# Performance work log

Measured on AMD Instinct MI355X. Metric: run time of the kernel, lower is better.

## Reference

```python
import jax, jax.numpy as jnp
import numpy as np

B, CIN, COUT, H, W = 4, 256, 256, 64, 64


def setup_inputs() -> dict:
    key = jax.random.key(0)
    ks = jax.random.split(key, 7)
    x = jax.random.normal(ks[0], (B, CIN, H, W), dtype=jnp.float32)
    s = 1.0 / np.sqrt(CIN)
    Wq = jax.random.uniform(ks[1], (COUT, CIN), jnp.float32, -s, s)
    Wk = jax.random.uniform(ks[2], (COUT, CIN), jnp.float32, -s, s)
    Wv = jax.random.uniform(ks[3], (COUT, CIN), jnp.float32, -s, s)
    bq = jax.random.uniform(ks[4], (COUT,), jnp.float32, -s, s)
    bk = jax.random.uniform(ks[5], (COUT,), jnp.float32, -s, s)
    bv = jax.random.uniform(ks[6], (COUT,), jnp.float32, -s, s)
    return {"x": x, "Wq": Wq, "Wk": Wk, "Wv": Wv, "bq": bq, "bk": bk, "bv": bv}


def reference(x, Wq, Wk, Wv, bq, bk, bv):
    b, cin, h, w = x.shape
    xf = x.reshape(b, cin, h * w)  # [B, Cin, N]
    # 1x1 conv == channel matmul
    q = jnp.einsum('oc,bcn->bon', Wq, xf) + bq[None, :, None]  # [B, C, N]
    k = jnp.einsum('oc,bcn->bon', Wk, xf) + bk[None, :, None]
    v = jnp.einsum('oc,bcn->bon', Wv, xf) + bv[None, :, None]
    # attention over flattened spatial positions (no 1/sqrt(d) scaling, as in source)
    scores = jnp.einsum('bcn,bcm->bnm', q, k)          # [B, N, N]
    attn = jax.nn.softmax(scores, axis=-1)
    out = jnp.einsum('bnm,bcm->bcn', attn, v)          # [B, C, N]
    return out.reshape(b, q.shape[1], h, w)
```

## Files before the change

### kernel.cpp

```cpp
#include <hip/hip_runtime.h>


typedef _Float16 f16;
typedef f16 f16x4 __attribute__((ext_vector_type(4)));
typedef f16 f16x8 __attribute__((ext_vector_type(8)));
typedef float f32x16 __attribute__((ext_vector_type(16)));

#define NB 4
#define NC 256
#define NN 4096
#define KVSPLIT 4
#define KRANGE (NN / KVSPLIT)
#define NCHUNK (KRANGE / 32)

typedef const __attribute__((address_space(1))) void* gas_t;
typedef __attribute__((address_space(3))) void* las_t;

__device__ __forceinline__ void load_lds16(const void* g, void* l) {
    __builtin_amdgcn_global_load_lds((gas_t)g, (las_t)l, 16, 0, 0);
}

__global__ __launch_bounds__(256) void wcvt_kernel(
    const float* __restrict__ Wq, const float* __restrict__ Wk,
    const float* __restrict__ Wv, f16* __restrict__ Wh)
{
    const int idx = blockIdx.x * 256 + threadIdx.x;
    const float* s = (idx < 65536) ? Wq : (idx < 131072 ? Wk : Wv);
    Wh[idx] = (f16)s[idx & 65535];
}

__global__ __launch_bounds__(256) void qkv_mfma_kernel(
    const float* __restrict__ x, const f16* __restrict__ Wh,
    const float* __restrict__ bq, const float* __restrict__ bk, const float* __restrict__ bv,
    f16* __restrict__ Qh, f16* __restrict__ Kh, f16* __restrict__ Vt)
{
    const int b  = blockIdx.y;
    const int n0 = blockIdx.x * 64;
    const int t  = threadIdx.x;
    const int wv = t >> 6, l = t & 63, ln = l & 31, g = l >> 5;

    __shared__ char xs[64 * 512];
    __shared__ char st[32768];

    {
        const int ci0 = t >> 4;
        const int nq  = (t & 15) * 4;
        for (int it = 0; it < 16; ++it) {
            const int ci = it * 16 + ci0;
            float v4[4];
            *(float4*)v4 = *(const float4*)(x + ((size_t)b * NC + ci) * NN + n0 + nq);
            const int gr = ci >> 3, lo = (ci & 7) * 2;
            #pragma unroll
            for (int j = 0; j < 4; ++j) {
                const int n = nq + j;
                *(f16*)(xs + n * 512 + ((gr ^ (n & 7)) * 16 + lo)) = (f16)v4[j];
            }
        }
    }
    __syncthreads();

    const int c0 = wv * 64;
    for (int m = 0; m < 3; ++m) {
        const f16*  W    = Wh + m * (NC * NC);
        const float* bias = (m == 0) ? bq : (m == 1 ? bk : bv);

        f32x16 acc[2][2];
        #pragma unroll
        for (int i = 0; i < 2; ++i)
            #pragma unroll
            for (int j = 0; j < 2; ++j)
                #pragma unroll
                for (int r = 0; r < 16; ++r) acc[i][j][r] = 0.0f;

        #pragma unroll
        for (int cs = 0; cs < 16; ++cs) {
            f16x8 a0 = *(const f16x8*)(W + (size_t)(c0 + ln) * NC + cs * 16 + 8 * g);
            f16x8 a1 = *(const f16x8*)(W + (size_t)(c0 + 32 + ln) * NC + cs * 16 + 8 * g);
            const int xb = (cs * 32 + g * 16) ^ ((ln & 7) << 4);
            f16x8 b0 = *(const f16x8*)(xs + ln * 512 + xb);
            f16x8 b1 = *(const f16x8*)(xs + (32 + ln) * 512 + xb);
            acc[0][0] = __builtin_amdgcn_mfma_f32_32x32x16_f16(a0, b0, acc[0][0], 0, 0, 0);
            acc[0][1] = __builtin_amdgcn_mfma_f32_32x32x16_f16(a0, b1, acc[0][1], 0, 0, 0);
            acc[1][0] = __builtin_amdgcn_mfma_f32_32x32x16_f16(a1, b0, acc[1][0], 0, 0, 0);
            acc[1][1] = __builtin_amdgcn_mfma_f32_32x32x16_f16(a1, b1, acc[1][1], 0, 0, 0);
        }

        __syncthreads();
        if (m < 2) {
            #pragma unroll
            for (int ct = 0; ct < 2; ++ct)
                #pragma unroll
                for (int nt = 0; nt < 2; ++nt)
                    #pragma unroll
                    for (int q = 0; q < 4; ++q) {
                        const int cb = c0 + ct * 32 + 8 * q + 4 * g;
                        f16x4 pk;
                        #pragma unroll
                        for (int j = 0; j < 4; ++j)
                            pk[j] = (f16)(acc[ct][nt][q * 4 + j] + bias[cb + j]);
                        const int n  = nt * 32 + ln;
                        const int g8 = cb >> 3;
                        *(f16x4*)(st + n * 512 + ((g8 ^ (n & 7)) * 16 + (cb & 7) * 2)) = pk;
                    }
            __syncthreads();
            f16* dst = (m == 0) ? Qh : Kh;
            const int gi  = t & 31;
            const int nb8 = (t >> 5) * 8;
            #pragma unroll
            for (int k = 0; k < 8; ++k) {
                const int n = nb8 + k;
                const uint4 d = *(const uint4*)(st + n * 512 + ((gi ^ (n & 7)) << 4));
                *(uint4*)(dst + ((size_t)b * NN + n0 + n) * NC + gi * 8) = d;
            }
        } else {
            #pragma unroll
            for (int ct = 0; ct < 2; ++ct)
                #pragma unroll
                for (int nt = 0; nt < 2; ++nt) {
                    const int n  = nt * 32 + ln;
                    const int pn = (n & ~15) | (n & 3) | ((n & 8) >> 1) | ((n & 4) << 1);
                    #pragma unroll
                    for (int r = 0; r < 16; ++r) {
                        const int c = c0 + ct * 32 + (r & 3) + 8 * (r >> 2) + 4 * g;
                        *(f16*)(st + c * 128 + ((pn * 2) ^ ((c & 7) << 4))) =
                            (f16)(acc[ct][nt][r] + bias[c]);
                    }
                }
            __syncthreads();
            #pragma unroll
            for (int ci = 0; ci < 8; ++ci) {
                const int c = ci * 32 + (t >> 3);
                const int s = t & 7;
                const uint4 d = *(const uint4*)(st + c * 128 + ((s ^ (c & 7)) << 4));
                *(uint4*)(Vt + ((size_t)b * NC + c) * NN + n0 + s * 8) = d;
            }
        }
    }
}

__global__ __launch_bounds__(256, 2) void flash_mfma_kernel(
    const f16* __restrict__ Qh, const f16* __restrict__ Kh, const f16* __restrict__ Vt,
    f16* __restrict__ Op, float* __restrict__ Mst, float* __restrict__ Lst)
{
    const int t  = threadIdx.x;
    const int wv = t >> 6;
    const int l  = t & 63;
    const int ln = l & 31;
    const int g  = l >> 5;

    const int flat  = blockIdx.x;
    const int xcd   = flat & 7;
    const int idx   = flat >> 3;
    const int bs    = xcd * 2 + (idx & 1);
    const int qt    = idx >> 1;
    const int b     = bs >> 2;
    const int split = bs & 3;
    const int qrow  = qt * 128 + wv * 32 + ln;

    __shared__ char ldsK[2 * 16384];
    __shared__ char ldsV[2 * 16384];

    f16x8 qf[16];
    {
        const f16* Qb = Qh + ((size_t)b * NN + qrow) * NC;
        #pragma unroll
        for (int cs = 0; cs < 16; ++cs)
            qf[cs] = *(const f16x8*)(Qb + cs * 16 + 8 * g);
    }

    f32x16 o[8];
    #pragma unroll
    for (int ct = 0; ct < 8; ++ct)
        #pragma unroll
        for (int r = 0; r < 16; ++r) o[ct][r] = 0.0f;

    float mrun = -1e30f, lrun = 0.0f;
    const int key_base = split * KRANGE;
    const f16* KhB = Kh + (size_t)b * NN * NC;
    const f16* VtB = Vt + (size_t)b * NC * NN;

#define DMA(CH, BUF) do {                                                            \
        const int key0_ = key_base + (CH) * 32;                                      \
        _Pragma("unroll")                                                            \
        for (int j = 0; j < 4; ++j) {                                                \
            const int r2  = wv * 4 + j;                                              \
            const int row = r2 * 2 + (l >> 5);                                       \
            const int u   = (l & 31) ^ (row & 15);                                   \
            load_lds16(KhB + (size_t)(key0_ + row) * NC + u * 8,                     \
                       ldsK + (BUF) * 16384 + r2 * 1024);                            \
        }                                                                            \
        _Pragma("unroll")                                                            \
        for (int j = 0; j < 4; ++j) {                                                \
            const int i  = wv * 4 + j;                                               \
            const int R  = i * 4 + (l >> 4);                                         \
            const int c  = R * 4 + ((l & 15) >> 2);                                  \
            const int kg = (l & 3) ^ (R & 3);                                        \
            load_lds16(VtB + (size_t)c * NN + key0_ + kg * 8,                        \
                       ldsV + (BUF) * 16384 + i * 1024);                             \
        }                                                                            \
    } while (0)

    DMA(0, 0);

    for (int ch = 0; ch < NCHUNK; ++ch) {
        const int cb = ch & 1;
        if (ch + 1 < NCHUNK) {
            DMA(ch + 1, cb ^ 1);
            asm volatile("s_waitcnt vmcnt(8)" ::: "memory");
        } else {
            asm volatile("s_waitcnt vmcnt(0)" ::: "memory");
        }
        __builtin_amdgcn_s_barrier();

        const char* K0 = ldsK + cb * 16384;
        const char* V0 = ldsV + cb * 16384;

        f32x16 s0;
        #pragma unroll
        for (int r = 0; r < 16; ++r) s0[r] = 0.0f;
        __builtin_amdgcn_s_setprio(1);
        #pragma unroll
        for (int cs = 0; cs < 16; ++cs) {
            const int col = ((cs * 2 + g) ^ (ln & 15)) * 16;
            f16x8 a0 = *(const f16x8*)(K0 + ln * 512 + col);
            s0 = __builtin_amdgcn_mfma_f32_32x32x16_f16(a0, qf[cs], s0, 0, 0, 0);
        }
        __builtin_amdgcn_s_setprio(0);

        float mt = s0[0];
        #pragma unroll
        for (int r = 1; r < 16; ++r) mt = fmaxf(mt, s0[r]);
        mt = fmaxf(mt, __shfl_xor(mt, 32));
        if (!__all(mt <= mrun + 8.0f)) {
            const float mnew  = fmaxf(mrun, mt);
            const float alpha = __expf(mrun - mnew);
            #pragma unroll
            for (int ct = 0; ct < 8; ++ct)
                #pragma unroll
                for (int r = 0; r < 16; ++r) o[ct][r] *= alpha;
            lrun *= alpha;
            mrun  = mnew;
        }

        float ps = 0.0f;
        f16x8 pf[2];
        #pragma unroll
        for (int r = 0; r < 16; ++r) {
            const float e0 = __expf(s0[r] - mrun);
            ps += e0;
            pf[r >> 3][r & 7] = (f16)e0;
        }
        ps += __shfl_xor(ps, 32);
        lrun += ps;

        __builtin_amdgcn_s_setprio(1);
        #pragma unroll
        for (int ct = 0; ct < 8; ++ct) {
            const int c    = ct * 32 + ln;
            const int base = (c >> 2) * 256 + (c & 3) * 64;
            const int rsw  = (c >> 2) & 3;
            #pragma unroll
            for (int s = 0; s < 2; ++s) {
                f16x8 va = *(const f16x8*)(V0 + base + (((s * 2 + g) ^ rsw) * 16));
                o[ct] = __builtin_amdgcn_mfma_f32_32x32x16_f16(va, pf[s], o[ct], 0, 0, 0);
            }
        }
        __builtin_amdgcn_s_setprio(0);

        __builtin_amdgcn_s_barrier();
    }
#undef DMA

    const float invl = 1.0f / lrun;
    #pragma unroll
    for (int ct = 0; ct < 8; ++ct)
        #pragma unroll
        for (int r = 0; r < 16; ++r) {
            const int c = ct * 32 + (r & 3) + 8 * (r >> 2) + 4 * g;
            Op[((size_t)(split * NB + b) * NC + c) * NN + qrow] = (f16)(o[ct][r] * invl);
        }
    if (g == 0) {
        Mst[(split * NB + b) * NN + qrow] = mrun;
        Lst[(split * NB + b) * NN + qrow] = lrun;
    }
}

__global__ __launch_bounds__(256) void combine_kernel(
    const f16* __restrict__ Op, const float* __restrict__ Mst, const float* __restrict__ Lst,
    float* __restrict__ out)
{
    const int t = threadIdx.x;
    const int b = blockIdx.y;
    const int n = blockIdx.x * 64 + (t & 63);

    float w[KVSPLIT];
    float mm = -1e30f;
    #pragma unroll
    for (int s = 0; s < KVSPLIT; ++s) {
        w[s] = Mst[(s * NB + b) * NN + n];
        mm = fmaxf(mm, w[s]);
    }
    float tot = 0.0f;
    #pragma unroll
    for (int s = 0; s < KVSPLIT; ++s) {
        w[s] = __expf(w[s] - mm) * Lst[(s * NB + b) * NN + n];
        tot += w[s];
    }
    const float inv = 1.0f / tot;
    #pragma unroll
    for (int s = 0; s < KVSPLIT; ++s) w[s] *= inv;

    for (int c = (t >> 6); c < NC; c += 4) {
        float acc = 0.0f;
        #pragma unroll
        for (int s = 0; s < KVSPLIT; ++s)
            acc += w[s] * (float)Op[((size_t)(s * NB + b) * NC + c) * NN + n];
        out[((size_t)b * NC + c) * NN + n] = acc;
    }
}

extern "C" void kernel_launch(void* const* d_in, const int* in_sizes, int n_in,
                              void* d_out, int out_size, void* d_ws, size_t ws_size,
                              hipStream_t stream)
{
    const float* x  = (const float*)d_in[0];
    const float* Wq = (const float*)d_in[1];
    const float* Wk = (const float*)d_in[2];
    const float* Wv = (const float*)d_in[3];
    const float* bq = (const float*)d_in[4];
    const float* bk = (const float*)d_in[5];
    const float* bv = (const float*)d_in[6];
    float* out = (float*)d_out;

    f16* Qh = (f16*)d_ws;
    f16* Kh = Qh + (size_t)NB * NN * NC;
    f16* Vt = Kh + (size_t)NB * NN * NC;
    f16* Op = Vt + (size_t)NB * NN * NC;
    float* Mst = (float*)(Op + (size_t)KVSPLIT * NB * NC * NN);
    float* Lst = Mst + (size_t)KVSPLIT * NB * NN;
    f16*  Wh  = (f16*)(Lst + (size_t)KVSPLIT * NB * NN);

    wcvt_kernel<<<768, 256, 0, stream>>>(Wq, Wk, Wv, Wh);
    qkv_mfma_kernel<<<dim3(NN / 64, NB), 256, 0, stream>>>(
        x, Wh, bq, bk, bv, Qh, Kh, Vt);
    flash_mfma_kernel<<<512, 256, 0, stream>>>(Qh, Kh, Vt, Op, Mst, Lst);
    combine_kernel<<<dim3(NN / 64, NB), 256, 0, stream>>>(Op, Mst, Lst, out);
}
```

Measured before the change: 136.0 us.

## Software-pipeline QK^T one chunk ahead of softmax/PV and use exp2 with prescaled Q

Restructures the attention main loop so the QK^T MFMAs for the next chunk are issued alongside the softmax and PV of the current chunk, using two score accumulators and split K/V DMA issue points. Separately folds log2(e) into Q during projection so the softmax uses exp2f instead of __expf, with the lazy-rescale threshold widened to 12 in the log2 domain. The combine kernel also switches to exp2f to match. The cost is higher register pressure from the extra score accumulator, and fp16 Q values are now scaled by 1.44, which slightly changes rounding.

```diff
diff --git a/kernel.cpp b/kernel.cpp
--- a/kernel.cpp
+++ b/kernel.cpp
@@ -63,6 +63,7 @@
     for (int m = 0; m < 3; ++m) {
         const f16*  W    = Wh + m * (NC * NC);
         const float* bias = (m == 0) ? bq : (m == 1 ? bk : bv);
+        const float qs   = (m == 0) ? 1.44269504f : 1.0f;
 
         f32x16 acc[2][2];
         #pragma unroll
@@ -97,7 +98,7 @@
                         f16x4 pk;
                         #pragma unroll
                         for (int j = 0; j < 4; ++j)
-                            pk[j] = (f16)(acc[ct][nt][q * 4 + j] + bias[cb + j]);
+                            pk[j] = (f16)((acc[ct][nt][q * 4 + j] + bias[cb + j]) * qs);
                         const int n  = nt * 32 + ln;
                         const int g8 = cb >> 3;
                         *(f16x4*)(st + n * 512 + ((g8 ^ (n & 7)) * 16 + (cb & 7) * 2)) = pk;
@@ -175,11 +176,12 @@
         for (int r = 0; r < 16; ++r) o[ct][r] = 0.0f;
 
     float mrun = -1e30f, lrun = 0.0f;
+    f16x8 pf[2];
     const int key_base = split * KRANGE;
     const f16* KhB = Kh + (size_t)b * NN * NC;
     const f16* VtB = Vt + (size_t)b * NC * NN;
 
-#define DMA(CH, BUF) do {                                                            \
+#define KDMA(CH, BUF) do {                                                           \
         const int key0_ = key_base + (CH) * 32;                                      \
         _Pragma("unroll")                                                            \
         for (int j = 0; j < 4; ++j) {                                                \
@@ -189,6 +191,10 @@
             load_lds16(KhB + (size_t)(key0_ + row) * NC + u * 8,                     \
                        ldsK + (BUF) * 16384 + r2 * 1024);                            \
         }                                                                            \
+    } while (0)
+
+#define VDMA(CH, BUF) do {                                                           \
+        const int key0_ = key_base + (CH) * 32;                                      \
         _Pragma("unroll")                                                            \
         for (int j = 0; j < 4; ++j) {                                                \
             const int i  = wv * 4 + j;                                               \
@@ -200,76 +206,96 @@
         }                                                                            \
     } while (0)
 
-    DMA(0, 0);
-
-    for (int ch = 0; ch < NCHUNK; ++ch) {
-        const int cb = ch & 1;
-        if (ch + 1 < NCHUNK) {
-            DMA(ch + 1, cb ^ 1);
-            asm volatile("s_waitcnt vmcnt(8)" ::: "memory");
-        } else {
-            asm volatile("s_waitcnt vmcnt(0)" ::: "memory");
-        }
-        __builtin_amdgcn_s_barrier();
-
-        const char* K0 = ldsK + cb * 16384;
-        const char* V0 = ldsV + cb * 16384;
-
-        f32x16 s0;
-        #pragma unroll
-        for (int r = 0; r < 16; ++r) s0[r] = 0.0f;
-        __builtin_amdgcn_s_setprio(1);
-        #pragma unroll
-        for (int cs = 0; cs < 16; ++cs) {
-            const int col = ((cs * 2 + g) ^ (ln & 15)) * 16;
-            f16x8 a0 = *(const f16x8*)(K0 + ln * 512 + col);
-            s0 = __builtin_amdgcn_mfma_f32_32x32x16_f16(a0, qf[cs], s0, 0, 0, 0);
-        }
-        __builtin_amdgcn_s_setprio(0);
-
-        float mt = s0[0];
-        #pragma unroll
-        for (int r = 1; r < 16; ++r) mt = fmaxf(mt, s0[r]);
-        mt = fmaxf(mt, __shfl_xor(mt, 32));
-        if (!__all(mt <= mrun + 8.0f)) {
-            const float mnew  = fmaxf(mrun, mt);
-            const float alpha = __expf(mrun - mnew);
-            #pragma unroll
-            for (int ct = 0; ct < 8; ++ct)
-                #pragma unroll
-                for (int r = 0; r < 16; ++r) o[ct][r] *= alpha;
-            lrun *= alpha;
-            mrun  = mnew;
-        }
-
-        float ps = 0.0f;
-        f16x8 pf[2];
-        #pragma unroll
-        for (int r = 0; r < 16; ++r) {
-            const float e0 = __expf(s0[r] - mrun);
-            ps += e0;
-            pf[r >> 3][r & 7] = (f16)e0;
-        }
-        ps += __shfl_xor(ps, 32);
-        lrun += ps;
-
-        __builtin_amdgcn_s_setprio(1);
-        #pragma unroll
-        for (int ct = 0; ct < 8; ++ct) {
-            const int c    = ct * 32 + ln;
-            const int base = (c >> 2) * 256 + (c & 3) * 64;
-            const int rsw  = (c >> 2) & 3;
-            #pragma unroll
-            for (int s = 0; s < 2; ++s) {
-                f16x8 va = *(const f16x8*)(V0 + base + (((s * 2 + g) ^ rsw) * 16));
-                o[ct] = __builtin_amdgcn_mfma_f32_32x32x16_f16(va, pf[s], o[ct], 0, 0, 0);
-            }
-        }
-        __builtin_amdgcn_s_setprio(0);
-
-        __builtin_amdgcn_s_barrier();
-    }
-#undef DMA
+#define QKC(BUF, SACC) do {                                                          \
+        _Pragma("unroll")                                                            \
+        for (int r = 0; r < 16; ++r) SACC[r] = 0.0f;                                 \
+        const char* K0_ = ldsK + (BUF) * 16384;                                      \
+        _Pragma("unroll")                                                            \
+        for (int cs = 0; cs < 16; ++cs) {                                            \
+            const int col = ((cs * 2 + g) ^ (ln & 15)) * 16;                         \
+            f16x8 a0 = *(const f16x8*)(K0_ + ln * 512 + col);                        \
+            SACC = __builtin_amdgcn_mfma_f32_32x32x16_f16(a0, qf[cs], SACC, 0, 0, 0);\
+        }                                                                            \
+    } while (0)
+
+#define SM(SP) do {                                                                  \
+        float mt = SP[0];                                                            \
+        _Pragma("unroll")                                                            \
+        for (int r = 1; r < 16; ++r) mt = fmaxf(mt, SP[r]);                          \
+        mt = fmaxf(mt, __shfl_xor(mt, 32));                                          \
+        if (!__all(mt <= mrun + 12.0f)) {                                            \
+            const float mnew  = fmaxf(mrun, mt);                                     \
+            const float alpha = exp2f(mrun - mnew);                                  \
+            _Pragma("unroll")                                                        \
+            for (int ct = 0; ct < 8; ++ct)                                           \
+                _Pragma("unroll")                                                    \
+                for (int r = 0; r < 16; ++r) o[ct][r] *= alpha;                      \
+            lrun *= alpha;                                                           \
+            mrun  = mnew;                                                            \
+        }                                                                            \
+        float ps = 0.0f;                                                             \
+        _Pragma("unroll")                                                            \
+        for (int r = 0; r < 16; ++r) {                                               \
+            const float e0 = exp2f(SP[r] - mrun);                                    \
+            ps += e0;                                                                \
+            pf[r >> 3][r & 7] = (f16)e0;                                             \
+        }                                                                            \
+        ps += __shfl_xor(ps, 32);                                                    \
+        lrun += ps;                                                                  \
+    } while (0)
+
+#define PVC(BUF) do {                                                                \
+        const char* V0_ = ldsV + (BUF) * 16384;                                      \
+        __builtin_amdgcn_s_setprio(1);                                               \
+        _Pragma("unroll")                                                            \
+        for (int ct = 0; ct < 8; ++ct) {                                             \
+            const int c    = ct * 32 + ln;                                           \
+            const int base = (c >> 2) * 256 + (c & 3) * 64;                          \
+            const int rsw  = (c >> 2) & 3;                                           \
+            _Pragma("unroll")                                                        \
+            for (int s = 0; s < 2; ++s) {                                            \
+                f16x8 va = *(const f16x8*)(V0_ + base + (((s * 2 + g) ^ rsw) * 16)); \
+                o[ct] = __builtin_amdgcn_mfma_f32_32x32x16_f16(va, pf[s], o[ct], 0, 0, 0); \
+            }                                                                        \
+        }                                                                            \
+        __builtin_amdgcn_s_setprio(0);                                               \
+    } while (0)
+
+#define STEP(SP, SC, BI, CH, PREF, DOQK, VM4) do {                                   \
+        if (VM4) asm volatile("s_waitcnt vmcnt(4)" ::: "memory");                    \
+        else     asm volatile("s_waitcnt vmcnt(0)" ::: "memory");                    \
+        __builtin_amdgcn_s_barrier();                                                \
+        if (PREF) KDMA((CH) + 2, BI);                                                \
+        if (DOQK) QKC((BI) ^ 1, SC);                                                 \
+        SM(SP);                                                                      \
+        PVC(BI);                                                                     \
+        __builtin_amdgcn_s_barrier();                                                \
+        if (PREF) VDMA((CH) + 2, BI);                                                \
+    } while (0)
+
+    f32x16 sA, sB;
+
+    KDMA(0, 0);
+    VDMA(0, 0);
+    KDMA(1, 1);
+    asm volatile("s_waitcnt vmcnt(8)" ::: "memory");
+    __builtin_amdgcn_s_barrier();
+    QKC(0, sA);
+    VDMA(1, 1);
+
+    for (int it = 0; it < NCHUNK - 2; it += 2) {
+        STEP(sA, sB, 0, it,     1, 1, 1);
+        STEP(sB, sA, 1, it + 1, 1, 1, 1);
+    }
+    STEP(sA, sB, 0, NCHUNK - 2, 0, 1, 1);
+    STEP(sB, sA, 1, NCHUNK - 1, 0, 0, 0);
+
+#undef STEP
+#undef PVC
+#undef SM
+#undef QKC
+#undef VDMA
+#undef KDMA
 
     const float invl = 1.0f / lrun;
     #pragma unroll
@@ -303,7 +329,7 @@
     float tot = 0.0f;
     #pragma unroll
     for (int s = 0; s < KVSPLIT; ++s) {
-        w[s] = __expf(w[s] - mm) * Lst[(s * NB + b) * NN + n];
+        w[s] = exp2f(w[s] - mm) * Lst[(s * NB + b) * NN + n];
         tot += w[s];
     }
     const float inv = 1.0f / tot;
```

New measurement: 248.4 us. +82.6%, slower.

## Fold log2e into Q, use exp2 softmax, split score accumulators, defer row-sum shuffle

Applied to the files above, without the earlier changes.

Scales Q by log2(e) in the projection epilogue so the attention softmax and the split combine can use exp2 directly instead of __expf. The QK^T MFMA chain is split into two independent accumulators to break the serial dependency, and the row max uses a tree reduction. The per-chunk cross-lane shuffle for the row sum is moved to a single shuffle after the loop, and the rescale threshold is widened from 8 to 12 in log2 units. The wider threshold lets unrescaled exponents grow larger before renormalisation, which raises fp16 overflow risk in P.

```diff
diff --git a/kernel.cpp b/kernel.cpp
--- a/kernel.cpp
+++ b/kernel.cpp
@@ -63,6 +63,7 @@
     for (int m = 0; m < 3; ++m) {
         const f16*  W    = Wh + m * (NC * NC);
         const float* bias = (m == 0) ? bq : (m == 1 ? bk : bv);
+        const float qs   = (m == 0) ? 1.44269504f : 1.0f;
 
         f32x16 acc[2][2];
         #pragma unroll
@@ -97,7 +98,7 @@
                         f16x4 pk;
                         #pragma unroll
                         for (int j = 0; j < 4; ++j)
-                            pk[j] = (f16)(acc[ct][nt][q * 4 + j] + bias[cb + j]);
+                            pk[j] = (f16)((acc[ct][nt][q * 4 + j] + bias[cb + j]) * qs);
                         const int n  = nt * 32 + ln;
                         const int g8 = cb >> 3;
                         *(f16x4*)(st + n * 512 + ((g8 ^ (n & 7)) * 16 + (cb & 7) * 2)) = pk;
@@ -215,25 +216,37 @@
         const char* K0 = ldsK + cb * 16384;
         const char* V0 = ldsV + cb * 16384;
 
-        f32x16 s0;
-        #pragma unroll
-        for (int r = 0; r < 16; ++r) s0[r] = 0.0f;
+        f32x16 sa, sb;
+        #pragma unroll
+        for (int r = 0; r < 16; ++r) { sa[r] = 0.0f; sb[r] = 0.0f; }
         __builtin_amdgcn_s_setprio(1);
         #pragma unroll
-        for (int cs = 0; cs < 16; ++cs) {
-            const int col = ((cs * 2 + g) ^ (ln & 15)) * 16;
-            f16x8 a0 = *(const f16x8*)(K0 + ln * 512 + col);
-            s0 = __builtin_amdgcn_mfma_f32_32x32x16_f16(a0, qf[cs], s0, 0, 0, 0);
+        for (int cs = 0; cs < 8; ++cs) {
+            const int colA = ((cs * 2 + g) ^ (ln & 15)) * 16;
+            const int colB = (((cs + 8) * 2 + g) ^ (ln & 15)) * 16;
+            f16x8 a0 = *(const f16x8*)(K0 + ln * 512 + colA);
+            f16x8 a1 = *(const f16x8*)(K0 + ln * 512 + colB);
+            sa = __builtin_amdgcn_mfma_f32_32x32x16_f16(a0, qf[cs],     sa, 0, 0, 0);
+            sb = __builtin_amdgcn_mfma_f32_32x32x16_f16(a1, qf[cs + 8], sb, 0, 0, 0);
         }
         __builtin_amdgcn_s_setprio(0);
 
-        float mt = s0[0];
-        #pragma unroll
-        for (int r = 1; r < 16; ++r) mt = fmaxf(mt, s0[r]);
-        mt = fmaxf(mt, __shfl_xor(mt, 32));
-        if (!__all(mt <= mrun + 8.0f)) {
+        float sv[16];
+        #pragma unroll
+        for (int r = 0; r < 16; ++r) sv[r] = sa[r] + sb[r];
+
+        float tm[16];
+        #pragma unroll
+        for (int r = 0; r < 16; ++r) tm[r] = sv[r];
+        #pragma unroll
+        for (int st = 8; st >= 1; st >>= 1)
+            #pragma unroll
+            for (int r = 0; r < st; ++r) tm[r] = fmaxf(tm[r], tm[r + st]);
+        float mt = fmaxf(tm[0], __shfl_xor(tm[0], 32));
+
+        if (!__all(mt <= mrun + 12.0f)) {
             const float mnew  = fmaxf(mrun, mt);
-            const float alpha = __expf(mrun - mnew);
+            const float alpha = exp2f(mrun - mnew);
             #pragma unroll
             for (int ct = 0; ct < 8; ++ct)
                 #pragma unroll
@@ -246,11 +259,10 @@
         f16x8 pf[2];
         #pragma unroll
         for (int r = 0; r < 16; ++r) {
-            const float e0 = __expf(s0[r] - mrun);
+            const float e0 = exp2f(sv[r] - mrun);
             ps += e0;
             pf[r >> 3][r & 7] = (f16)e0;
         }
-        ps += __shfl_xor(ps, 32);
         lrun += ps;
 
         __builtin_amdgcn_s_setprio(1);
@@ -271,6 +283,7 @@
     }
 #undef DMA
 
+    lrun += __shfl_xor(lrun, 32);
     const float invl = 1.0f / lrun;
     #pragma unroll
     for (int ct = 0; ct < 8; ++ct)
@@ -303,7 +316,7 @@
     float tot = 0.0f;
     #pragma unroll
     for (int s = 0; s < KVSPLIT; ++s) {
-        w[s] = __expf(w[s] - mm) * Lst[(s * NB + b) * NN + n];
+        w[s] = exp2f(w[s] - mm) * Lst[(s * NB + b) * NN + n];
         tot += w[s];
     }
     const float inv = 1.0f / tot;
```

Result: slower. 167.7 us (+23.3%).
